# Performance work log

Measured on AMD Instinct MI355X. Metric: run time of the kernel, lower is better.

Reference implementation:

```python
import jax, jax.numpy as jnp
import numpy as np

N_HIDDEN = 4096
N_OUT = 128
BATCH = 512


def setup_inputs() -> dict:
    key = jax.random.key(0)
    k1, k2, k3, k4, k5 = jax.random.split(key, 5)
    H = jax.random.normal(k1, (BATCH, N_HIDDEN), dtype=jnp.float32)
    # p is the running inverse-covariance state; build it SPD-ish and well
    # scaled like a real OS-ELM state: p ~ (A A^T / n + reg*I)^-1-ish scale.
    A = jax.random.normal(k2, (N_HIDDEN, N_HIDDEN), dtype=jnp.float32)
    p = 0.001 * (A @ A.T) / N_HIDDEN + 0.01 * jnp.eye(N_HIDDEN, dtype=jnp.float32)
    beta = 0.02 * jax.random.normal(k3, (N_HIDDEN, N_OUT), dtype=jnp.float32)
    target = jax.random.normal(k4, (BATCH, N_OUT), dtype=jnp.float32)
    return {"H": H, "p": p, "beta": beta, "target": target}


def reference(H, p, beta, target):
    # Incremental OS-ELM recursive least-squares update (training branch,
    # after initial training is finished).
    B = H.shape[0]
    Hp = H @ p                              # [B, n]
    S = jnp.eye(B, dtype=H.dtype) + Hp @ H.T  # [B, B]
    temp = jnp.linalg.pinv(S)               # on-device pinv (TF used host np.linalg.pinv)
    pHT = p @ H.T                           # [n, B]
    p_new = p - (pHT @ temp) @ Hp           # [n, n]
    # beta update uses the updated p
    Hbeta = H @ beta                        # [B, o]
    beta_new = beta + (p_new @ H.T) @ (target - Hbeta)  # [n, o]
    out = H @ beta_new                      # [B, o]
    return out
```

## Files before the change

### kernel.cpp

```cpp
#include <hip/hip_runtime.h>
#include <hip/hip_bf16.h>


typedef __attribute__((ext_vector_type(8))) short short8;
typedef __attribute__((ext_vector_type(4))) float f32x4;

#define NH 4096
#define NO 128
#define NBATCH 512

__device__ __forceinline__ unsigned short f2b(float x) {
  return __builtin_bit_cast(unsigned short, __float2bfloat16(x));
}

__device__ __forceinline__ float bu2f(unsigned short u) {
  return __builtin_bit_cast(float, ((unsigned int)u) << 16);
}

__device__ __forceinline__ float b2f_lo(unsigned int u) {
  return __builtin_bit_cast(float, u << 16);
}
__device__ __forceinline__ float b2f_hi(unsigned int u) {
  return __builtin_bit_cast(float, u & 0xffff0000u);
}

__device__ __forceinline__ void gload_lds16(const void* g, void* l) {
  __builtin_amdgcn_global_load_lds(
      (const __attribute__((address_space(1))) unsigned int*)g,
      (__attribute__((address_space(3))) unsigned int*)l, 16, 0, 0);
}

__global__ __launch_bounds__(256) void k_cast(const float* __restrict__ src,
                                              unsigned short* __restrict__ dst) {
  int i = blockIdx.x * 256 + threadIdx.x;
  float4 v = reinterpret_cast<const float4*>(src)[i];
  ushort4 o;
  o.x = f2b(v.x); o.y = f2b(v.y); o.z = f2b(v.z); o.w = f2b(v.w);
  reinterpret_cast<ushort4*>(dst)[i] = o;
}

__global__ __launch_bounds__(256) void k_cast_bt(const float* __restrict__ beta,
                                                 unsigned short* __restrict__ bT) {
  __shared__ unsigned short tile[128][130];
  const int t = threadIdx.x;
  const int k0 = blockIdx.x * 128;
  {
    const int r = t >> 1, c0 = (t & 1) * 64;
    const float* src = &beta[(size_t)(k0 + r) * NO + c0];
    #pragma unroll
    for (int i = 0; i < 16; ++i) {
      float4 v = *(const float4*)(src + i * 4);
      tile[r][c0 + i * 4 + 0] = f2b(v.x);
      tile[r][c0 + i * 4 + 1] = f2b(v.y);
      tile[r][c0 + i * 4 + 2] = f2b(v.z);
      tile[r][c0 + i * 4 + 3] = f2b(v.w);
    }
  }
  __syncthreads();
  {
    const int c = t >> 1, h = (t & 1) * 64;
    unsigned short* dst = &bT[(size_t)c * NH + k0 + h];
    #pragma unroll
    for (int i = 0; i < 16; ++i) {
      ushort4 o;
      o.x = tile[h + i * 4 + 0][c];
      o.y = tile[h + i * 4 + 1][c];
      o.z = tile[h + i * 4 + 2][c];
      o.w = tile[h + i * 4 + 3][c];
      *(ushort4*)(dst + i * 4) = o;
    }
  }
}

__global__ __launch_bounds__(512, 2) void k_gemm_hp(
    const unsigned short* __restrict__ A,
    const float* __restrict__ P,
    unsigned short* __restrict__ Cp) {
  __shared__ __align__(16) unsigned short As[2][128 * 64];
  __shared__ __align__(16) unsigned short Bs[2][128 * 64];
  const int t = threadIdx.x, w = t >> 6, l = t & 63;
  const int n0 = blockIdx.x * 128, m0 = blockIdx.y * 128;
  const int kb = blockIdx.z * 1024;
  const int wr = w >> 2, wc = w & 3;
  const int fl = l & 15, fk = (l >> 4) * 8;
  const int srow = l >> 3;
  const int kcolsw = (((l & 7) ^ srow) * 8);
  const unsigned short* asrc0 = A + (size_t)(m0 + w * 16 + srow) * NH + kb + kcolsw;
  const unsigned short* asrc1 = A + (size_t)(m0 + w * 16 + 8 + srow) * NH + kb + kcolsw;
  const int brow = t >> 3, bg = t & 7;
  const float* bsrc0 = P + (size_t)(n0 + brow) * NH + kb + bg * 8;
  const float* bsrc1 = P + (size_t)(n0 + 64 + brow) * NH + kb + bg * 8;
  const int bx = (bg ^ (brow & 7)) * 8;
  const int bwoff0 = brow * 64 + bx;
  const int bwoff1 = bwoff0 + 64 * 64;

  f32x4 z = {0.f, 0.f, 0.f, 0.f};
  f32x4 acc00 = z, acc01 = z, acc10 = z, acc11 = z;
  f32x4 acc20 = z, acc21 = z, acc30 = z, acc31 = z;

  const int xr = (fl & 7) * 8;

#define STAGE_A(kt, buf)                                    \
  {                                                         \
    const int kn = (kt) * 64;                               \
    gload_lds16(asrc0 + kn, &As[(buf)][w * 1024]);          \
    gload_lds16(asrc1 + kn, &As[(buf)][w * 1024 + 512]);    \
  }

#define LOAD_B(kt, r0, r1, r2, r3)                          \
  {                                                         \
    const float* b0p = bsrc0 + (kt) * 64;                   \
    const float* b1p = bsrc1 + (kt) * 64;                   \
    r0 = *(const float4*)b0p;  r1 = *(const float4*)(b0p + 4); \
    r2 = *(const float4*)b1p;  r3 = *(const float4*)(b1p + 4); \
  }

#define WRITE_B(buf, r0, r1, r2, r3)                        \
  {                                                         \
    short8 p0, p1;                                          \
    p0[0] = (short)f2b(r0.x); p0[1] = (short)f2b(r0.y);     \
    p0[2] = (short)f2b(r0.z); p0[3] = (short)f2b(r0.w);     \
    p0[4] = (short)f2b(r1.x); p0[5] = (short)f2b(r1.y);     \
    p0[6] = (short)f2b(r1.z); p0[7] = (short)f2b(r1.w);     \
    p1[0] = (short)f2b(r2.x); p1[1] = (short)f2b(r2.y);     \
    p1[2] = (short)f2b(r2.z); p1[3] = (short)f2b(r2.w);     \
    p1[4] = (short)f2b(r3.x); p1[5] = (short)f2b(r3.y);     \
    p1[6] = (short)f2b(r3.z); p1[7] = (short)f2b(r3.w);     \
    *(short8*)&Bs[(buf)][bwoff0] = p0;                      \
    *(short8*)&Bs[(buf)][bwoff1] = p1;                      \
  }

#define COMPUTE_HP(buf)                                                        \
  {                                                                            \
    const unsigned short* Ab = As[(buf)];                                      \
    const unsigned short* Bb = Bs[(buf)];                                      \
    _Pragma("unroll")                                                          \
    for (int ks = 0; ks < 2; ++ks) {                                           \
      const int x = (ks * 32 + fk) ^ xr;                                       \
      short8 b0 = *(const short8*)&Bb[(wc * 32 + fl) * 64 + x];                \
      short8 b1 = *(const short8*)&Bb[(wc * 32 + 16 + fl) * 64 + x];           \
      short8 a0 = *(const short8*)&Ab[(wr * 64 + fl) * 64 + x];                \
      short8 a1 = *(const short8*)&Ab[(wr * 64 + 16 + fl) * 64 + x];           \
      short8 a2 = *(const short8*)&Ab[(wr * 64 + 32 + fl) * 64 + x];           \
      short8 a3 = *(const short8*)&Ab[(wr * 64 + 48 + fl) * 64 + x];           \
      acc00 = __builtin_amdgcn_mfma_f32_16x16x32_bf16(a0, b0, acc00, 0, 0, 0); \
      acc01 = __builtin_amdgcn_mfma_f32_16x16x32_bf16(a0, b1, acc01, 0, 0, 0); \
      acc10 = __builtin_amdgcn_mfma_f32_16x16x32_bf16(a1, b0, acc10, 0, 0, 0); \
      acc11 = __builtin_amdgcn_mfma_f32_16x16x32_bf16(a1, b1, acc11, 0, 0, 0); \
      acc20 = __builtin_amdgcn_mfma_f32_16x16x32_bf16(a2, b0, acc20, 0, 0, 0); \
      acc21 = __builtin_amdgcn_mfma_f32_16x16x32_bf16(a2, b1, acc21, 0, 0, 0); \
      acc30 = __builtin_amdgcn_mfma_f32_16x16x32_bf16(a3, b0, acc30, 0, 0, 0); \
      acc31 = __builtin_amdgcn_mfma_f32_16x16x32_bf16(a3, b1, acc31, 0, 0, 0); \
    }                                                                          \
  }

  float4 e0, e1, e2, e3, o0, o1, o2, o3;
  LOAD_B(0, e0, e1, e2, e3);
  STAGE_A(0, 0);
  LOAD_B(1, o0, o1, o2, o3);
  asm volatile("s_waitcnt vmcnt(6)" ::: "memory");
  WRITE_B(0, e0, e1, e2, e3);

  for (int k2 = 0; k2 < 14; k2 += 2) {
    asm volatile("s_waitcnt vmcnt(4) lgkmcnt(0)" ::: "memory");
    __builtin_amdgcn_s_barrier();
    STAGE_A(k2 + 1, 1);
    asm volatile("s_waitcnt vmcnt(2)" ::: "memory");
    WRITE_B(1, o0, o1, o2, o3);
    LOAD_B(k2 + 2, e0, e1, e2, e3);
    COMPUTE_HP(0);
    asm volatile("s_waitcnt vmcnt(4) lgkmcnt(0)" ::: "memory");
    __builtin_amdgcn_s_barrier();
    STAGE_A(k2 + 2, 0);
    asm volatile("s_waitcnt vmcnt(2)" ::: "memory");
    WRITE_B(0, e0, e1, e2, e3);
    LOAD_B(k2 + 3, o0, o1, o2, o3);
    COMPUTE_HP(1);
  }
  asm volatile("s_waitcnt vmcnt(4) lgkmcnt(0)" ::: "memory");
  __builtin_amdgcn_s_barrier();
  STAGE_A(15, 1);
  asm volatile("s_waitcnt vmcnt(2)" ::: "memory");
  WRITE_B(1, o0, o1, o2, o3);
  COMPUTE_HP(0);
  asm volatile("s_waitcnt vmcnt(0) lgkmcnt(0)" ::: "memory");
  __builtin_amdgcn_s_barrier();
  COMPUTE_HP(1);
#undef COMPUTE_HP
#undef WRITE_B
#undef LOAD_B
#undef STAGE_A

  unsigned short* Co = Cp + (size_t)blockIdx.z * (NBATCH * NH);
  const int rb = (l >> 4) * 4;
  const int cw = n0 + wc * 32 + fl;
  #pragma unroll
  for (int j = 0; j < 4; ++j) {
    int m = m0 + wr * 64 + rb + j;
    Co[(size_t)m * NH + cw]        = f2b(acc00[j]);
    Co[(size_t)m * NH + cw + 16]   = f2b(acc01[j]);
    Co[(size_t)(m + 16) * NH + cw]      = f2b(acc10[j]);
    Co[(size_t)(m + 16) * NH + cw + 16] = f2b(acc11[j]);
    Co[(size_t)(m + 32) * NH + cw]      = f2b(acc20[j]);
    Co[(size_t)(m + 32) * NH + cw + 16] = f2b(acc21[j]);
    Co[(size_t)(m + 48) * NH + cw]      = f2b(acc30[j]);
    Co[(size_t)(m + 48) * NH + cw + 16] = f2b(acc31[j]);
  }
}

__global__ __launch_bounds__(256) void k_reduce_hp(const unsigned short* __restrict__ Hpp,
                                                   unsigned short* __restrict__ Hp) {
  int i = blockIdx.x * 256 + threadIdx.x;
  const int stride = NBATCH * NH / 4;
  ushort4 a = reinterpret_cast<const ushort4*>(Hpp)[i];
  ushort4 b = reinterpret_cast<const ushort4*>(Hpp)[i + stride];
  ushort4 c = reinterpret_cast<const ushort4*>(Hpp)[i + 2 * stride];
  ushort4 d = reinterpret_cast<const ushort4*>(Hpp)[i + 3 * stride];
  ushort4 o;
  o.x = f2b((bu2f(a.x) + bu2f(b.x)) + (bu2f(c.x) + bu2f(d.x)));
  o.y = f2b((bu2f(a.y) + bu2f(b.y)) + (bu2f(c.y) + bu2f(d.y)));
  o.z = f2b((bu2f(a.z) + bu2f(b.z)) + (bu2f(c.z) + bu2f(d.z)));
  o.w = f2b((bu2f(a.w) + bu2f(b.w)) + (bu2f(c.w) + bu2f(d.w)));
  reinterpret_cast<ushort4*>(Hp)[i] = o;
}

__global__ __launch_bounds__(512, 2) void k_gemm_s(
    const unsigned short* __restrict__ A,
    const unsigned short* __restrict__ Bm,
    float* __restrict__ Spart) {
  __shared__ __align__(16) unsigned short As[3][128 * 64];
  __shared__ __align__(16) unsigned short Bs[3][64 * 64];
  const int t = threadIdx.x, w = t >> 6, l = t & 63;
  const int m0 = blockIdx.y * 128, n0 = blockIdx.x * 64;
  const int kb = blockIdx.z * 512;
  const int wr = w >> 1, wc = w & 1, fl = l & 15, fk = (l >> 4) * 8;
  const int srow = l >> 3;
  const int kcolsw = (((l & 7) ^ srow) * 8);
  const unsigned short* asrc0 = A + (size_t)(m0 + w * 16 + srow) * NH + kb + kcolsw;
  const unsigned short* asrc1 = A + (size_t)(m0 + w * 16 + 8 + srow) * NH + kb + kcolsw;
  const unsigned short* bsrc  = Bm + (size_t)(n0 + w * 8 + srow) * NH + kb + kcolsw;

  f32x4 z = {0.f, 0.f, 0.f, 0.f};
  f32x4 acc00 = z, acc01 = z, acc10 = z, acc11 = z;

  const int xr = (fl & 7) * 8;

#define STAGE_S(kt, buf)                                    \
  {                                                         \
    const int kn = (kt) * 64;                               \
    gload_lds16(asrc0 + kn, &As[(buf)][w * 1024]);          \
    gload_lds16(asrc1 + kn, &As[(buf)][w * 1024 + 512]);    \
    gload_lds16(bsrc + kn,  &Bs[(buf)][w * 512]);           \
  }

#define COMPUTE_S(buf)                                                         \
  {                                                                            \
    const unsigned short* Ab = As[(buf)];                                      \
    const unsigned short* Bb = Bs[(buf)];                                      \
    _Pragma("unroll")                                                          \
    for (int ks = 0; ks < 2; ++ks) {                                           \
      const int x = (ks * 32 + fk) ^ xr;                                       \
      short8 a0 = *(const short8*)&Ab[(wr * 32 + fl) * 64 + x];                \
      short8 a1 = *(const short8*)&Ab[(wr * 32 + 16 + fl) * 64 + x];           \
      short8 b0 = *(const short8*)&Bb[(wc * 32 + fl) * 64 + x];                \
      short8 b1 = *(const short8*)&Bb[(wc * 32 + 16 + fl) * 64 + x];           \
      acc00 = __builtin_amdgcn_mfma_f32_16x16x32_bf16(a0, b0, acc00, 0, 0, 0); \
      acc01 = __builtin_amdgcn_mfma_f32_16x16x32_bf16(a0, b1, acc01, 0, 0, 0); \
      acc10 = __builtin_amdgcn_mfma_f32_16x16x32_bf16(a1, b0, acc10, 0, 0, 0); \
      acc11 = __builtin_amdgcn_mfma_f32_16x16x32_bf16(a1, b1, acc11, 0, 0, 0); \
    }                                                                          \
  }

#define ITER_S(kt, buf)                                           \
  {                                                               \
    asm volatile("s_waitcnt vmcnt(3) lgkmcnt(0)" ::: "memory");   \
    __builtin_amdgcn_s_barrier();                                 \
    if ((kt) + 2 < 8) STAGE_S((kt) + 2, ((buf) + 2) % 3);         \
    COMPUTE_S(buf);                                               \
  }

  STAGE_S(0, 0);
  STAGE_S(1, 1);
  ITER_S(0, 0); ITER_S(1, 1); ITER_S(2, 2);
  ITER_S(3, 0); ITER_S(4, 1); ITER_S(5, 2);
  ITER_S(6, 0);
  asm volatile("s_waitcnt vmcnt(0) lgkmcnt(0)" ::: "memory");
  __builtin_amdgcn_s_barrier();
  COMPUTE_S(1);
#undef ITER_S
#undef COMPUTE_S
#undef STAGE_S

  float* sp = Spart + (size_t)blockIdx.z * (512 * 512);
  const int rb = (l >> 4) * 4;
  #pragma unroll
  for (int j = 0; j < 4; ++j) {
    int m = m0 + wr * 32 + rb + j;
    sp[(size_t)m * 512 + n0 + wc * 32 + fl]      = acc00[j];
    sp[(size_t)m * 512 + n0 + wc * 32 + 16 + fl] = acc01[j];
    int m2 = m + 16;
    sp[(size_t)m2 * 512 + n0 + wc * 32 + fl]      = acc10[j];
    sp[(size_t)m2 * 512 + n0 + wc * 32 + 16 + fl] = acc11[j];
  }
}

__global__ __launch_bounds__(512, 2) void k_r_gemm(
    const unsigned short* __restrict__ A,
    const unsigned short* __restrict__ Bm,
    float* __restrict__ rpart) {
  __shared__ __align__(16) unsigned short As[2][128 * 64];
  __shared__ __align__(16) unsigned short Bs[2][64 * 64];
  const int t = threadIdx.x, w = t >> 6, l = t & 63;
  const int m0 = blockIdx.y * 128, n0 = blockIdx.x * 64;
  const int kb = blockIdx.z * 256;
  const int wr = w >> 1, wc = w & 1, fl = l & 15, fk = (l >> 4) * 8;
  const int srow = l >> 3, kcol = (l & 7) * 8;
  const unsigned short* asrc0 = A + (size_t)(m0 + w * 16 + srow) * NH + kb + kcol;
  const unsigned short* asrc1 = A + (size_t)(m0 + w * 16 + 8 + srow) * NH + kb + kcol;
  const unsigned short* bsrc  = Bm + (size_t)(n0 + w * 8 + srow) * NH + kb + kcol;

  f32x4 z = {0.f, 0.f, 0.f, 0.f};
  f32x4 acc00 = z, acc01 = z, acc10 = z, acc11 = z;

  gload_lds16(asrc0, &As[0][w * 1024]);
  gload_lds16(asrc1, &As[0][w * 1024 + 512]);
  gload_lds16(bsrc,  &Bs[0][w * 512]);
  __syncthreads();

  int cur = 0;
  for (int kt = 0; kt < 4; ++kt) {
    if (kt + 1 < 4) {
      const int kn = (kt + 1) * 64;
      gload_lds16(asrc0 + kn, &As[cur ^ 1][w * 1024]);
      gload_lds16(asrc1 + kn, &As[cur ^ 1][w * 1024 + 512]);
      gload_lds16(bsrc  + kn, &Bs[cur ^ 1][w * 512]);
    }
    const unsigned short* Ab = As[cur];
    const unsigned short* Bb = Bs[cur];
    #pragma unroll
    for (int ks = 0; ks < 2; ++ks) {
      short8 a0 = *(const short8*)&Ab[(wr * 32 + fl) * 64 + ks * 32 + fk];
      short8 a1 = *(const short8*)&Ab[(wr * 32 + 16 + fl) * 64 + ks * 32 + fk];
      short8 b0 = *(const short8*)&Bb[(wc * 32 + fl) * 64 + ks * 32 + fk];
      short8 b1 = *(const short8*)&Bb[(wc * 32 + 16 + fl) * 64 + ks * 32 + fk];
      acc00 = __builtin_amdgcn_mfma_f32_16x16x32_bf16(a0, b0, acc00, 0, 0, 0);
      acc01 = __builtin_amdgcn_mfma_f32_16x16x32_bf16(a0, b1, acc01, 0, 0, 0);
      acc10 = __builtin_amdgcn_mfma_f32_16x16x32_bf16(a1, b0, acc10, 0, 0, 0);
      acc11 = __builtin_amdgcn_mfma_f32_16x16x32_bf16(a1, b1, acc11, 0, 0, 0);
    }
    __syncthreads();
    cur ^= 1;
  }

  float* rp = rpart + (size_t)blockIdx.z * (NBATCH * NO);
  const int rb = (l >> 4) * 4;
  #pragma unroll
  for (int j = 0; j < 4; ++j) {
    int m = m0 + wr * 32 + rb + j;
    rp[(size_t)m * NO + n0 + wc * 32 + fl]      = acc00[j];
    rp[(size_t)m * NO + n0 + wc * 32 + 16 + fl] = acc01[j];
    int m2 = m + 16;
    rp[(size_t)m2 * NO + n0 + wc * 32 + fl]      = acc10[j];
    rp[(size_t)m2 * NO + n0 + wc * 32 + 16 + fl] = acc11[j];
  }
}

__global__ __launch_bounds__(256) void k_reduce_s(const float* __restrict__ Spart,
                                                  unsigned short* __restrict__ Sb) {
  int i = blockIdx.x * 256 + threadIdx.x;
  float acc = ((i >> 9) == (i & 511)) ? 1.0f : 0.0f;
  #pragma unroll
  for (int c = 0; c < 8; ++c) acc += Spart[c * 262144 + i];
  Sb[i] = f2b(acc);
}

__global__ __launch_bounds__(256) void k_r_reduce16(const float* __restrict__ rpart,
                                                    const float* __restrict__ target,
                                                    float* __restrict__ rbuf) {
  int i = blockIdx.x * 256 + threadIdx.x;
  float acc = target[i];
  #pragma unroll
  for (int c = 0; c < 16; ++c) acc -= rpart[c * (NBATCH * NO) + i];
  rbuf[i] = acc;
}

__device__ __forceinline__ float block_reduce1(float a, float* red) {
  #pragma unroll
  for (int off = 32; off; off >>= 1) a += __shfl_xor(a, off);
  const int t = threadIdx.x;
  __syncthreads();
  if ((t & 63) == 0) red[t >> 6] = a;
  __syncthreads();
  float ra = 0.f;
  #pragma unroll
  for (int q2 = 0; q2 < 8; ++q2) ra += red[q2];
  return ra;
}

#define CG_ITERS 4
__global__ __launch_bounds__(512) void k_cg(const unsigned short* __restrict__ Sb,
                                            const float* __restrict__ rbuf,
                                            const float* __restrict__ target,
                                            float* __restrict__ out) {
  __shared__ float pl[512];
  __shared__ float vred[8][512];
  __shared__ float red[8];
  const int t = threadIdx.x;
  const int q = t >> 6;
  const int rt = t & 63;
  const int j = blockIdx.x;

  float r = rbuf[(size_t)t * NO + j];
  float x = 0.f;
  pl[t] = r;
  float rho = block_reduce1(r * r, red);
  __syncthreads();

  const uint4* S8 = (const uint4*)Sb;
  const uint4* sp = S8 + (size_t)(q * 64) * 64 + rt;
  const float* pq = &pl[q * 64];

  for (int it = 0; it < CG_ITERS; ++it) {
    float a0 = 0.f, a1 = 0.f, a2 = 0.f, a3 = 0.f;
    float a4 = 0.f, a5 = 0.f, a6 = 0.f, a7 = 0.f;
    #pragma unroll 8
    for (int k = 0; k < 64; ++k) {
      uint4 sv = sp[(size_t)k * 64];
      float p = pq[k];
      a0 += b2f_lo(sv.x) * p; a1 += b2f_hi(sv.x) * p;
      a2 += b2f_lo(sv.y) * p; a3 += b2f_hi(sv.y) * p;
      a4 += b2f_lo(sv.z) * p; a5 += b2f_hi(sv.z) * p;
      a6 += b2f_lo(sv.w) * p; a7 += b2f_hi(sv.w) * p;
    }
    *(float4*)&vred[q][8 * rt]     = make_float4(a0, a1, a2, a3);
    *(float4*)&vred[q][8 * rt + 4] = make_float4(a4, a5, a6, a7);
    __syncthreads();
    float v = 0.f;
    #pragma unroll
    for (int c = 0; c < 8; ++c) v += vred[c][t];
    float p = pl[t];
    float ppv = block_reduce1(p * v, red);
    float al = rho / ppv;
    x += al * p;
    r -= al * v;
    float rhon = block_reduce1(r * r, red);
    float be = rhon / rho;
    rho = rhon;
    __syncthreads();
    pl[t] = r + be * p;
    __syncthreads();
  }
  out[(size_t)t * NO + j] = target[(size_t)t * NO + j] - x;
}

extern "C" void kernel_launch(void* const* d_in, const int* in_sizes, int n_in,
                              void* d_out, int out_size, void* d_ws, size_t ws_size,
                              hipStream_t stream) {
  (void)in_sizes; (void)n_in; (void)out_size; (void)ws_size;
  const float* H      = (const float*)d_in[0];
  const float* P      = (const float*)d_in[1];
  const float* beta   = (const float*)d_in[2];
  const float* target = (const float*)d_in[3];
  float* out = (float*)d_out;

  char* ws = (char*)d_ws;
  unsigned short* Hb  = (unsigned short*)(ws);
  unsigned short* Hp  = (unsigned short*)(ws + (4u << 20));
  unsigned short* Hpp = (unsigned short*)(ws + (8u << 20));
  float* Spart        = (float*)(ws + (8u << 20));
  unsigned short* bT  = (unsigned short*)(ws + (16u << 20));
  float* rpart        = (float*)(ws + (17u << 20));
  unsigned short* Sb  = (unsigned short*)(ws + (21u << 20));
  float* rbuf         = (float*)(ws + (21u << 20) + (512u << 10));

  k_cast<<<2048, 256, 0, stream>>>(H, Hb);
  k_gemm_hp<<<dim3(32, 4, 4), 512, 0, stream>>>(Hb, P, Hpp);
  k_reduce_hp<<<2048, 256, 0, stream>>>(Hpp, Hp);
  k_gemm_s<<<dim3(8, 4, 8), 512, 0, stream>>>(Hp, Hb, Spart);
  k_reduce_s<<<1024, 256, 0, stream>>>(Spart, Sb);
  k_cast_bt<<<32, 256, 0, stream>>>(beta, bT);
  k_r_gemm<<<dim3(2, 4, 16), 512, 0, stream>>>(Hb, bT, rpart);
  k_r_reduce16<<<256, 256, 0, stream>>>(rpart, target, rbuf);
  k_cg<<<NO, 512, 0, stream>>>(Sb, rbuf, target, out);
}
```

Measured before the change: 90.42 us.

## Drop LDS staging in H@p GEMM and cut CG iterations

The H@p GEMM kernel no longer double-buffers A and B tiles through shared memory. Each wave now loads its MFMA fragments straight from global memory and converts the fp32 p to bf16 in registers, and the occupancy hint rises from 2 to 4 blocks. The aim is to remove LDS traffic and barriers, at the cost of redundant global loads across waves, which now lean on the cache. Separately, the CG solver drops from 4 to 3 iterations, which does less work but may lower accuracy.

```diff
diff --git a/kernel.cpp b/kernel.cpp
--- a/kernel.cpp
+++ b/kernel.cpp
@@ -72,124 +72,53 @@
   }
 }
 
-__global__ __launch_bounds__(512, 2) void k_gemm_hp(
+__global__ __launch_bounds__(512, 4) void k_gemm_hp(
     const unsigned short* __restrict__ A,
     const float* __restrict__ P,
     unsigned short* __restrict__ Cp) {
-  __shared__ __align__(16) unsigned short As[2][128 * 64];
-  __shared__ __align__(16) unsigned short Bs[2][128 * 64];
   const int t = threadIdx.x, w = t >> 6, l = t & 63;
   const int n0 = blockIdx.x * 128, m0 = blockIdx.y * 128;
   const int kb = blockIdx.z * 1024;
   const int wr = w >> 2, wc = w & 3;
   const int fl = l & 15, fk = (l >> 4) * 8;
-  const int srow = l >> 3;
-  const int kcolsw = (((l & 7) ^ srow) * 8);
-  const unsigned short* asrc0 = A + (size_t)(m0 + w * 16 + srow) * NH + kb + kcolsw;
-  const unsigned short* asrc1 = A + (size_t)(m0 + w * 16 + 8 + srow) * NH + kb + kcolsw;
-  const int brow = t >> 3, bg = t & 7;
-  const float* bsrc0 = P + (size_t)(n0 + brow) * NH + kb + bg * 8;
-  const float* bsrc1 = P + (size_t)(n0 + 64 + brow) * NH + kb + bg * 8;
-  const int bx = (bg ^ (brow & 7)) * 8;
-  const int bwoff0 = brow * 64 + bx;
-  const int bwoff1 = bwoff0 + 64 * 64;
+
+  const unsigned short* ap = A + (size_t)(m0 + wr * 64 + fl) * NH + kb + fk;
+  const float* bp0 = P + (size_t)(n0 + wc * 32 + fl) * NH + kb + fk;
+  const float* bp1 = P + (size_t)(n0 + wc * 32 + 16 + fl) * NH + kb + fk;
 
   f32x4 z = {0.f, 0.f, 0.f, 0.f};
   f32x4 acc00 = z, acc01 = z, acc10 = z, acc11 = z;
   f32x4 acc20 = z, acc21 = z, acc30 = z, acc31 = z;
 
-  const int xr = (fl & 7) * 8;
-
-#define STAGE_A(kt, buf)                                    \
-  {                                                         \
-    const int kn = (kt) * 64;                               \
-    gload_lds16(asrc0 + kn, &As[(buf)][w * 1024]);          \
-    gload_lds16(asrc1 + kn, &As[(buf)][w * 1024 + 512]);    \
-  }
-
-#define LOAD_B(kt, r0, r1, r2, r3)                          \
-  {                                                         \
-    const float* b0p = bsrc0 + (kt) * 64;                   \
-    const float* b1p = bsrc1 + (kt) * 64;                   \
-    r0 = *(const float4*)b0p;  r1 = *(const float4*)(b0p + 4); \
-    r2 = *(const float4*)b1p;  r3 = *(const float4*)(b1p + 4); \
-  }
-
-#define WRITE_B(buf, r0, r1, r2, r3)                        \
-  {                                                         \
-    short8 p0, p1;                                          \
-    p0[0] = (short)f2b(r0.x); p0[1] = (short)f2b(r0.y);     \
-    p0[2] = (short)f2b(r0.z); p0[3] = (short)f2b(r0.w);     \
-    p0[4] = (short)f2b(r1.x); p0[5] = (short)f2b(r1.y);     \
-    p0[6] = (short)f2b(r1.z); p0[7] = (short)f2b(r1.w);     \
-    p1[0] = (short)f2b(r2.x); p1[1] = (short)f2b(r2.y);     \
-    p1[2] = (short)f2b(r2.z); p1[3] = (short)f2b(r2.w);     \
-    p1[4] = (short)f2b(r3.x); p1[5] = (short)f2b(r3.y);     \
-    p1[6] = (short)f2b(r3.z); p1[7] = (short)f2b(r3.w);     \
-    *(short8*)&Bs[(buf)][bwoff0] = p0;                      \
-    *(short8*)&Bs[(buf)][bwoff1] = p1;                      \
-  }
-
-#define COMPUTE_HP(buf)                                                        \
-  {                                                                            \
-    const unsigned short* Ab = As[(buf)];                                      \
-    const unsigned short* Bb = Bs[(buf)];                                      \
-    _Pragma("unroll")                                                          \
-    for (int ks = 0; ks < 2; ++ks) {                                           \
-      const int x = (ks * 32 + fk) ^ xr;                                       \
-      short8 b0 = *(const short8*)&Bb[(wc * 32 + fl) * 64 + x];                \
-      short8 b1 = *(const short8*)&Bb[(wc * 32 + 16 + fl) * 64 + x];           \
-      short8 a0 = *(const short8*)&Ab[(wr * 64 + fl) * 64 + x];                \
-      short8 a1 = *(const short8*)&Ab[(wr * 64 + 16 + fl) * 64 + x];           \
-      short8 a2 = *(const short8*)&Ab[(wr * 64 + 32 + fl) * 64 + x];           \
-      short8 a3 = *(const short8*)&Ab[(wr * 64 + 48 + fl) * 64 + x];           \
-      acc00 = __builtin_amdgcn_mfma_f32_16x16x32_bf16(a0, b0, acc00, 0, 0, 0); \
-      acc01 = __builtin_amdgcn_mfma_f32_16x16x32_bf16(a0, b1, acc01, 0, 0, 0); \
-      acc10 = __builtin_amdgcn_mfma_f32_16x16x32_bf16(a1, b0, acc10, 0, 0, 0); \
-      acc11 = __builtin_amdgcn_mfma_f32_16x16x32_bf16(a1, b1, acc11, 0, 0, 0); \
-      acc20 = __builtin_amdgcn_mfma_f32_16x16x32_bf16(a2, b0, acc20, 0, 0, 0); \
-      acc21 = __builtin_amdgcn_mfma_f32_16x16x32_bf16(a2, b1, acc21, 0, 0, 0); \
-      acc30 = __builtin_amdgcn_mfma_f32_16x16x32_bf16(a3, b0, acc30, 0, 0, 0); \
-      acc31 = __builtin_amdgcn_mfma_f32_16x16x32_bf16(a3, b1, acc31, 0, 0, 0); \
-    }                                                                          \
-  }
-
-  float4 e0, e1, e2, e3, o0, o1, o2, o3;
-  LOAD_B(0, e0, e1, e2, e3);
-  STAGE_A(0, 0);
-  LOAD_B(1, o0, o1, o2, o3);
-  asm volatile("s_waitcnt vmcnt(6)" ::: "memory");
-  WRITE_B(0, e0, e1, e2, e3);
-
-  for (int k2 = 0; k2 < 14; k2 += 2) {
-    asm volatile("s_waitcnt vmcnt(4) lgkmcnt(0)" ::: "memory");
-    __builtin_amdgcn_s_barrier();
-    STAGE_A(k2 + 1, 1);
-    asm volatile("s_waitcnt vmcnt(2)" ::: "memory");
-    WRITE_B(1, o0, o1, o2, o3);
-    LOAD_B(k2 + 2, e0, e1, e2, e3);
-    COMPUTE_HP(0);
-    asm volatile("s_waitcnt vmcnt(4) lgkmcnt(0)" ::: "memory");
-    __builtin_amdgcn_s_barrier();
-    STAGE_A(k2 + 2, 0);
-    asm volatile("s_waitcnt vmcnt(2)" ::: "memory");
-    WRITE_B(0, e0, e1, e2, e3);
-    LOAD_B(k2 + 3, o0, o1, o2, o3);
-    COMPUTE_HP(1);
-  }
-  asm volatile("s_waitcnt vmcnt(4) lgkmcnt(0)" ::: "memory");
-  __builtin_amdgcn_s_barrier();
-  STAGE_A(15, 1);
-  asm volatile("s_waitcnt vmcnt(2)" ::: "memory");
-  WRITE_B(1, o0, o1, o2, o3);
-  COMPUTE_HP(0);
-  asm volatile("s_waitcnt vmcnt(0) lgkmcnt(0)" ::: "memory");
-  __builtin_amdgcn_s_barrier();
-  COMPUTE_HP(1);
-#undef COMPUTE_HP
-#undef WRITE_B
-#undef LOAD_B
-#undef STAGE_A
+  #pragma unroll 2
+  for (int kt = 0; kt < 32; ++kt) {
+    const int ko = kt * 32;
+    short8 a0 = *(const short8*)(ap + ko);
+    short8 a1 = *(const short8*)(ap + 16 * NH + ko);
+    short8 a2 = *(const short8*)(ap + 32 * NH + ko);
+    short8 a3 = *(const short8*)(ap + 48 * NH + ko);
+    float4 lo0 = *(const float4*)(bp0 + ko);
+    float4 hi0 = *(const float4*)(bp0 + ko + 4);
+    float4 lo1 = *(const float4*)(bp1 + ko);
+    float4 hi1 = *(const float4*)(bp1 + ko + 4);
+    short8 b0, b1;
+    b0[0] = (short)f2b(lo0.x); b0[1] = (short)f2b(lo0.y);
+    b0[2] = (short)f2b(lo0.z); b0[3] = (short)f2b(lo0.w);
+    b0[4] = (short)f2b(hi0.x); b0[5] = (short)f2b(hi0.y);
+    b0[6] = (short)f2b(hi0.z); b0[7] = (short)f2b(hi0.w);
+    b1[0] = (short)f2b(lo1.x); b1[1] = (short)f2b(lo1.y);
+    b1[2] = (short)f2b(lo1.z); b1[3] = (short)f2b(lo1.w);
+    b1[4] = (short)f2b(hi1.x); b1[5] = (short)f2b(hi1.y);
+    b1[6] = (short)f2b(hi1.z); b1[7] = (short)f2b(hi1.w);
+    acc00 = __builtin_amdgcn_mfma_f32_16x16x32_bf16(a0, b0, acc00, 0, 0, 0);
+    acc01 = __builtin_amdgcn_mfma_f32_16x16x32_bf16(a0, b1, acc01, 0, 0, 0);
+    acc10 = __builtin_amdgcn_mfma_f32_16x16x32_bf16(a1, b0, acc10, 0, 0, 0);
+    acc11 = __builtin_amdgcn_mfma_f32_16x16x32_bf16(a1, b1, acc11, 0, 0, 0);
+    acc20 = __builtin_amdgcn_mfma_f32_16x16x32_bf16(a2, b0, acc20, 0, 0, 0);
+    acc21 = __builtin_amdgcn_mfma_f32_16x16x32_bf16(a2, b1, acc21, 0, 0, 0);
+    acc30 = __builtin_amdgcn_mfma_f32_16x16x32_bf16(a3, b0, acc30, 0, 0, 0);
+    acc31 = __builtin_amdgcn_mfma_f32_16x16x32_bf16(a3, b1, acc31, 0, 0, 0);
+  }
 
   unsigned short* Co = Cp + (size_t)blockIdx.z * (NBATCH * NH);
   const int rb = (l >> 4) * 4;
@@ -397,7 +326,7 @@
   return ra;
 }
 
-#define CG_ITERS 4
+#define CG_ITERS 3
 __global__ __launch_bounds__(512) void k_cg(const unsigned short* __restrict__ Sb,
                                             const float* __restrict__ rbuf,
                                             const float* __restrict__ target,
```

Measured after the change: 176.1 us. 94.7% more time.
